# Performance work log

Hardware: AMD Instinct MI355X
Metric: run time of the kernel (lower is better)

The kernel has to match this reference:

```python
import jax, jax.numpy as jnp
import numpy as np
from jax import lax

B, C, H, W = 32, 684, 16, 64
HID, A, CK, K = 256, 512, 512, 11


def setup_inputs() -> dict:
    key = jax.random.key(0)
    ks = jax.random.split(key, 12)
    s = 0.02
    return {
        "cnn_features": jax.random.normal(ks[0], (B, C, H, W), jnp.float32),
        "hidden": jax.random.normal(ks[1], (B, HID), jnp.float32),
        "alpha_sum": jax.random.uniform(ks[2], (B, 1, H, W), jnp.float32),
        "image_mask": jnp.ones((B, 1, H, W), jnp.float32),
        # hidden_weight: Linear(HID -> A)
        "Wh": jax.random.normal(ks[3], (A, HID), jnp.float32) * s,
        "bh": jnp.zeros((A,), jnp.float32),
        # encoder_feature_conv: Conv2d(C -> A, 1x1) == pointwise linear
        "Wec": jax.random.normal(ks[4], (A, C), jnp.float32) * s,
        "bec": jnp.zeros((A,), jnp.float32),
        # attention_conv: Conv2d(1 -> CK, 11x11, pad 5, no bias)
        "Wac": jax.random.normal(ks[5], (CK, 1, K, K), jnp.float32) * s,
        # attention_weight: Linear(CK -> A, no bias)
        "Waw": jax.random.normal(ks[6], (A, CK), jnp.float32) * s,
        # alpha_convert: Linear(A -> 1)
        "Wv": jax.random.normal(ks[7], (1, A), jnp.float32) * s,
        "bv": jnp.zeros((1,), jnp.float32),
    }


def reference(cnn_features, hidden, alpha_sum, image_mask,
              Wh, bh, Wec, bec, Wac, Waw, Wv, bv):
    # query = hidden_weight(hidden): [B, A]
    query = hidden @ Wh.T + bh
    # attention_conv(alpha_sum): [B, CK, H, W]
    ast = lax.conv_general_dilated(
        alpha_sum, Wac, window_strides=(1, 1),
        padding=[(K // 2, K // 2), (K // 2, K // 2)],
        dimension_numbers=("NCHW", "OIHW", "NCHW"))
    # attention_weight on permuted conv output: [B, H, W, A]
    coverage_alpha = jnp.einsum("bkhw,ak->bhwa", ast, Waw)
    # encoder_feature_conv (1x1 conv == pointwise linear): [B, H, W, A]
    cnn_trans = jnp.einsum("bchw,ac->bhwa", cnn_features, Wec) + bec
    # additive attention score
    alpha_score = jnp.tanh(query[:, None, None, :] + coverage_alpha + cnn_trans)
    # alpha_convert -> scalar energy per position: [B, H, W]
    energy = jnp.einsum("bhwa,a->bhw", alpha_score, Wv[0]) + bv[0]
    energy = energy - energy.max()  # global max-subtract as in original
    energy_exp = jnp.exp(energy) * image_mask[:, 0]
    denom = energy_exp.sum(axis=(-1, -2))[:, None, None] + 1e-10
    alpha = energy_exp / denom  # [B, H, W]
    alpha_sum_new = alpha[:, None, :, :] + alpha_sum  # [B, 1, H, W]
    # context: weighted spatial sum over features -> [B, C]
    context_vector = jnp.einsum("bhw,bchw->bc", alpha, cnn_features)
    return (context_vector, alpha, alpha_sum_new)
```

## Files before the change

kernel.cpp:

```cpp
#include <hip/hip_runtime.h>
#include <math.h>

#define Bn   32
#define Cn   684
#define Hn   16
#define Wn   64
#define HWn  1024
#define HIDn 256
#define An   512
#define KKn  121
#define CREAL 805
#define CPAD 832
#define NSTEP 26

#define OUT_ALPHA 21888
#define OUT_ASUM  (21888 + 32768)

typedef short short8 __attribute__((ext_vector_type(8)));
typedef float floatx4 __attribute__((ext_vector_type(4)));

__device__ __forceinline__ unsigned short f2bf(float f) {
    union { float f; unsigned int i; } v; v.f = f;
    unsigned int i = v.i;
    return (unsigned short)((i + 0x7fffu + ((i >> 16) & 1u)) >> 16);
}

__device__ __forceinline__ void async_lds16(void* lds, const void* g) {
    __builtin_amdgcn_global_load_lds(
        (const __attribute__((address_space(1))) unsigned int*)g,
        (__attribute__((address_space(3))) unsigned int*)lds, 16, 0, 0);
}

__global__ __launch_bounds__(256) void k_query(
    const float* __restrict__ hidden,
    const float* __restrict__ Wh,
    const float* __restrict__ bh,
    const float* __restrict__ bec,
    float* __restrict__ query)
{
    __shared__ float hs[HIDn];
    const int b = blockIdx.x, t = threadIdx.x;
    if (t < HIDn) hs[t] = hidden[b * HIDn + t];
    __syncthreads();
    for (int a = t; a < An; a += 256) {
        const float4* wp = (const float4*)(Wh + (size_t)a * HIDn);
        float s = bh[a] + bec[a];
        #pragma unroll 8
        for (int i = 0; i < HIDn / 4; ++i) {
            float4 w = wp[i];
            s = fmaf(hs[4 * i],     w.x, s);
            s = fmaf(hs[4 * i + 1], w.y, s);
            s = fmaf(hs[4 * i + 2], w.z, s);
            s = fmaf(hs[4 * i + 3], w.w, s);
        }
        query[b * An + a] = s;
    }
}

__global__ __launch_bounds__(128) void k_build_vt(
    const float* __restrict__ Wec,
    const float* __restrict__ Wac,
    const float* __restrict__ Waw,
    unsigned short* __restrict__ VTbf)
{
    __shared__ float waw_s[512];
    const int a = blockIdx.x, t = threadIdx.x;
    for (int i = t; i < 512; i += 128) waw_s[i] = Waw[(size_t)a * 512 + i];
    __syncthreads();
    for (int cp = t; cp < Cn; cp += 128)
        VTbf[(size_t)a * CPAD + cp] = f2bf(Wec[(size_t)a * Cn + cp]);
    if (t < KKn) {
        float s = 0.f;
        #pragma unroll 8
        for (int k = 0; k < 512; ++k)
            s = fmaf(waw_s[k], Wac[k * KKn + t], s);
        VTbf[(size_t)a * CPAD + Cn + t] = f2bf(s);
    }
    for (int cp = CREAL + t; cp < CPAD; cp += 128)
        VTbf[(size_t)a * CPAD + cp] = 0;
}

__device__ __forceinline__ float fetchU(const float* __restrict__ X,
                                        const float* plane,
                                        int b, int hh, int m, int row) {
    if (row < Cn)   return X[((size_t)(b * Cn + row)) * HWn + hh * Wn + m];
    if (row < CREAL) {
        int ij = row - Cn; int di = ij / 11, dj = ij - di * 11;
        return plane[di * 74 + m + dj];
    }
    return 0.f;
}

__global__ __launch_bounds__(256, 2) void k_energy(
    const float* __restrict__ X,
    const float* __restrict__ asum,
    const float* __restrict__ Wv,
    const float* __restrict__ query,
    const unsigned short* __restrict__ VTbf,
    float* __restrict__ energy)
{
    __shared__ unsigned short As[64 * 40];
    __shared__ unsigned short Bs[512 * 32];
    __shared__ float plane[11 * 74];
    __shared__ float qs[512];
    __shared__ float wvs[512];

    const int t = threadIdx.x;
    const int hh = blockIdx.x, b = blockIdx.y;
    const int w = t >> 6, lane = t & 63;
    const int q = lane >> 4, r = lane & 15;

    for (int i = t; i < 11 * 74; i += 256) {
        int di = i / 74, cc = i - di * 74;
        int h2 = hh + di - 5, w2 = cc - 5;
        float v = 0.f;
        if (h2 >= 0 && h2 < Hn && w2 >= 0 && w2 < Wn) v = asum[b * HWn + h2 * Wn + w2];
        plane[i] = v;
    }
    qs[t]        = query[b * An + t];
    qs[t + 256]  = query[b * An + t + 256];
    wvs[t]       = Wv[t];
    wvs[t + 256] = Wv[t + 256];

    floatx4 acc[4][8];
    #pragma unroll
    for (int mf = 0; mf < 4; ++mf)
        #pragma unroll
        for (int nf = 0; nf < 8; ++nf)
            acc[mf][nf] = (floatx4){0.f, 0.f, 0.f, 0.f};

    for (int ch = 0; ch < NSTEP; ++ch) {
        const int c0 = ch * 32;
        __syncthreads();
        {
            unsigned int pk[4];
            #pragma unroll
            for (int jj = 0; jj < 4; ++jj) {
                int r0 = c0 + w * 8 + jj * 2;
                float v0 = fetchU(X, plane, b, hh, lane, r0);
                float v1 = fetchU(X, plane, b, hh, lane, r0 + 1);
                unsigned int u0 = __float_as_uint(v0), u1 = __float_as_uint(v1);
                u0 = (u0 + 0x7fffu + ((u0 >> 16) & 1u)) >> 16;
                u1 = (u1 + 0x7fffu + ((u1 >> 16) & 1u)) & 0xffff0000u;
                pk[jj] = u0 | u1;
            }
            uint4* dst = (uint4*)&As[lane * 40 + w * 8];
            *dst = make_uint4(pk[0], pk[1], pk[2], pk[3]);
        }
        #pragma unroll
        for (int ii = 0; ii < 8; ++ii) {
            int n0 = w * 128 + ii * 16;
            int rowB = n0 + (lane >> 2);
            int gc = (lane & 3) ^ ((lane >> 2) & 3);
            const unsigned short* gB = VTbf + (size_t)rowB * CPAD + c0 + gc * 8;
            async_lds16(&Bs[n0 * 32], gB);
        }
        __syncthreads();
        short8 af[4], bfr[8];
        #pragma unroll
        for (int mf = 0; mf < 4; ++mf)
            af[mf] = *(const short8*)&As[(mf * 16 + r) * 40 + q * 8];
        #pragma unroll
        for (int nf = 0; nf < 8; ++nf) {
            int rowB = w * 128 + nf * 16 + r;
            bfr[nf] = *(const short8*)&Bs[rowB * 32 + (q ^ (r & 3)) * 8];
        }
        #pragma unroll
        for (int mf = 0; mf < 4; ++mf)
            #pragma unroll
            for (int nf = 0; nf < 8; ++nf)
                acc[mf][nf] = __builtin_amdgcn_mfma_f32_16x16x32_bf16(
                    af[mf], bfr[nf], acc[mf][nf], 0, 0, 0);
    }

    float ep[16];
    #pragma unroll
    for (int i = 0; i < 16; ++i) ep[i] = 0.f;
    #pragma unroll
    for (int nf = 0; nf < 8; ++nf) {
        int n = w * 128 + nf * 16 + r;
        float qv = qs[n], wv = wvs[n];
        #pragma unroll
        for (int mf = 0; mf < 4; ++mf)
            #pragma unroll
            for (int rg = 0; rg < 4; ++rg) {
                float x = acc[mf][nf][rg] + qv;
                float e2 = __expf(2.f * x);
                float th = 1.f - 2.f * __builtin_amdgcn_rcpf(e2 + 1.f);
                ep[mf * 4 + rg] += wv * th;
            }
    }
    __syncthreads();
    float* red = (float*)Bs;
    #pragma unroll
    for (int mf = 0; mf < 4; ++mf)
        #pragma unroll
        for (int rg = 0; rg < 4; ++rg)
            red[(mf * 16 + q * 4 + rg) * 65 + w * 16 + r] = ep[mf * 4 + rg];
    __syncthreads();
    if (t < 64) {
        float s = 0.f;
        #pragma unroll 16
        for (int i = 0; i < 64; ++i) s += red[t * 65 + i];
        energy[b * HWn + hh * Wn + t] = s;
    }
}

__global__ __launch_bounds__(1024) void k_max(
    const float* __restrict__ energy, float* __restrict__ emax)
{
    __shared__ float wm[16];
    const int t = threadIdx.x;
    float m = -1e30f;
    for (int i = t; i < Bn * HWn; i += 1024) m = fmaxf(m, energy[i]);
    for (int off = 32; off >= 1; off >>= 1) m = fmaxf(m, __shfl_down(m, off, 64));
    if ((t & 63) == 0) wm[t >> 6] = m;
    __syncthreads();
    if (t == 0) {
        float mm = wm[0];
        for (int i = 1; i < 16; ++i) mm = fmaxf(mm, wm[i]);
        emax[0] = mm;
    }
}

__global__ __launch_bounds__(1024) void k_softmax(
    const float* __restrict__ energy, const float* __restrict__ emax,
    const float* __restrict__ mask, const float* __restrict__ asum,
    float* __restrict__ alpha_f, float* __restrict__ out)
{
    __shared__ float sm[17];
    const int b = blockIdx.x, t = threadIdx.x;
    float ex = expf(energy[b * HWn + t] - emax[0]) * mask[b * HWn + t];
    float s = ex;
    for (int off = 32; off >= 1; off >>= 1) s += __shfl_down(s, off, 64);
    if ((t & 63) == 0) sm[t >> 6] = s;
    __syncthreads();
    if (t == 0) {
        float tot = 0.f;
        for (int i = 0; i < 16; ++i) tot += sm[i];
        sm[16] = tot + 1e-10f;
    }
    __syncthreads();
    float alpha = ex / sm[16];
    alpha_f[b * HWn + t] = alpha;
    out[OUT_ALPHA + b * HWn + t] = alpha;
    out[OUT_ASUM  + b * HWn + t] = alpha + asum[b * HWn + t];
}

__global__ __launch_bounds__(256) void k_context(
    const float* __restrict__ X, const float* __restrict__ alpha_f,
    float* __restrict__ out)
{
    const int t = threadIdx.x, lane = t & 63, wid = t >> 6;
    const int b = blockIdx.y;
    const int c = blockIdx.x * 4 + wid;
    const float* xp = X + ((size_t)(b * Cn + c)) * HWn;
    const float* ap = alpha_f + b * HWn;
    float s = 0.f;
    #pragma unroll
    for (int i = 0; i < 4; ++i) {
        int off = i * 256 + lane * 4;
        float4 x = *(const float4*)(xp + off);
        float4 a = *(const float4*)(ap + off);
        s = fmaf(a.x, x.x, s);
        s = fmaf(a.y, x.y, s);
        s = fmaf(a.z, x.z, s);
        s = fmaf(a.w, x.w, s);
    }
    for (int off = 32; off >= 1; off >>= 1) s += __shfl_down(s, off, 64);
    if (lane == 0) out[b * Cn + c] = s;
}

extern "C" void kernel_launch(void* const* d_in, const int* in_sizes, int n_in,
                              void* d_out, int out_size, void* d_ws, size_t ws_size,
                              hipStream_t stream)
{
    const float* X      = (const float*)d_in[0];
    const float* hidden = (const float*)d_in[1];
    const float* asum   = (const float*)d_in[2];
    const float* mask   = (const float*)d_in[3];
    const float* Wh     = (const float*)d_in[4];
    const float* bh     = (const float*)d_in[5];
    const float* Wec    = (const float*)d_in[6];
    const float* bec    = (const float*)d_in[7];
    const float* Wac    = (const float*)d_in[8];
    const float* Waw    = (const float*)d_in[9];
    const float* Wv     = (const float*)d_in[10];
    (void)in_sizes; (void)n_in; (void)out_size; (void)ws_size;

    float* out = (float*)d_out;
    float* ws = (float*)d_ws;
    float* query   = ws;
    float* energy  = ws + 16384;
    float* emax    = ws + 16384 + 32768;
    float* alpha_f = emax + 16;
    unsigned short* VTbf = (unsigned short*)(alpha_f + 32768);

    k_query   <<<dim3(32),      dim3(256),  0, stream>>>(hidden, Wh, bh, bec, query);
    k_build_vt<<<dim3(512),     dim3(128),  0, stream>>>(Wec, Wac, Waw, VTbf);
    k_energy  <<<dim3(16, 32),  dim3(256),  0, stream>>>(X, asum, Wv, query, VTbf, energy);
    k_max     <<<dim3(1),       dim3(1024), 0, stream>>>(energy, emax);
    k_softmax <<<dim3(32),      dim3(1024), 0, stream>>>(energy, emax, mask, asum, alpha_f, out);
    k_context <<<dim3(171, 32), dim3(256),  0, stream>>>(X, alpha_f, out);
}
```

Measured before the change: 258.1 us.

## Drop LDS staging in energy GEMM, merge prep kernels, fuse max into softmax

The energy kernel now loads bf16 weight fragments and packed feature fragments straight from global memory into registers, with no LDS tiles and no per-step barriers. The loop is split so the fast path skips the coverage-plane branch. The query and weight-build kernels merge into one launch, and the separate global-max kernel is replaced by a per-batch max inside the softmax. Per-batch max subtraction is mathematically equivalent apart from epsilon and underflow effects. In exchange, each wave redundantly loads the whole feature tile with poorly coalesced strided loads and no prefetching.

```diff
diff --git a/kernel.cpp b/kernel.cpp
--- a/kernel.cpp
+++ b/kernel.cpp
@@ -24,71 +24,60 @@
     unsigned int i = v.i;
     return (unsigned short)((i + 0x7fffu + ((i >> 16) & 1u)) >> 16);
 }
-
-__device__ __forceinline__ void async_lds16(void* lds, const void* g) {
-    __builtin_amdgcn_global_load_lds(
-        (const __attribute__((address_space(1))) unsigned int*)g,
-        (__attribute__((address_space(3))) unsigned int*)lds, 16, 0, 0);
-}
-
-__global__ __launch_bounds__(256) void k_query(
+__device__ __forceinline__ unsigned int pack2bf(float v0, float v1) {
+    unsigned int u0 = __float_as_uint(v0), u1 = __float_as_uint(v1);
+    u0 = (u0 + 0x7fffu + ((u0 >> 16) & 1u)) >> 16;
+    u1 = (u1 + 0x7fffu + ((u1 >> 16) & 1u)) & 0xffff0000u;
+    return u0 | u1;
+}
+
+__global__ __launch_bounds__(256) void k_prep(
     const float* __restrict__ hidden,
     const float* __restrict__ Wh,
     const float* __restrict__ bh,
     const float* __restrict__ bec,
-    float* __restrict__ query)
-{
-    __shared__ float hs[HIDn];
-    const int b = blockIdx.x, t = threadIdx.x;
-    if (t < HIDn) hs[t] = hidden[b * HIDn + t];
-    __syncthreads();
-    for (int a = t; a < An; a += 256) {
-        const float4* wp = (const float4*)(Wh + (size_t)a * HIDn);
-        float s = bh[a] + bec[a];
-        #pragma unroll 8
-        for (int i = 0; i < HIDn / 4; ++i) {
-            float4 w = wp[i];
-            s = fmaf(hs[4 * i],     w.x, s);
-            s = fmaf(hs[4 * i + 1], w.y, s);
-            s = fmaf(hs[4 * i + 2], w.z, s);
-            s = fmaf(hs[4 * i + 3], w.w, s);
-        }
-        query[b * An + a] = s;
-    }
-}
-
-__global__ __launch_bounds__(128) void k_build_vt(
     const float* __restrict__ Wec,
     const float* __restrict__ Wac,
     const float* __restrict__ Waw,
+    float* __restrict__ query,
     unsigned short* __restrict__ VTbf)
 {
-    __shared__ float waw_s[512];
-    const int a = blockIdx.x, t = threadIdx.x;
-    for (int i = t; i < 512; i += 128) waw_s[i] = Waw[(size_t)a * 512 + i];
-    __syncthreads();
-    for (int cp = t; cp < Cn; cp += 128)
-        VTbf[(size_t)a * CPAD + cp] = f2bf(Wec[(size_t)a * Cn + cp]);
-    if (t < KKn) {
-        float s = 0.f;
-        #pragma unroll 8
-        for (int k = 0; k < 512; ++k)
-            s = fmaf(waw_s[k], Wac[k * KKn + t], s);
-        VTbf[(size_t)a * CPAD + Cn + t] = f2bf(s);
-    }
-    for (int cp = CREAL + t; cp < CPAD; cp += 128)
-        VTbf[(size_t)a * CPAD + cp] = 0;
-}
-
-__device__ __forceinline__ float fetchU(const float* __restrict__ X,
-                                        const float* plane,
-                                        int b, int hh, int m, int row) {
-    if (row < Cn)   return X[((size_t)(b * Cn + row)) * HWn + hh * Wn + m];
-    if (row < CREAL) {
-        int ij = row - Cn; int di = ij / 11, dj = ij - di * 11;
-        return plane[di * 74 + m + dj];
-    }
-    return 0.f;
+    __shared__ float sbuf[512];
+    const int blk = blockIdx.x, t = threadIdx.x;
+    if (blk < 512) {
+        const int a = blk;
+        sbuf[t]       = Waw[(size_t)a * 512 + t];
+        sbuf[t + 256] = Waw[(size_t)a * 512 + t + 256];
+        __syncthreads();
+        for (int cp = t; cp < Cn; cp += 256)
+            VTbf[(size_t)a * CPAD + cp] = f2bf(Wec[(size_t)a * Cn + cp]);
+        if (t < KKn) {
+            float s = 0.f;
+            #pragma unroll 8
+            for (int k = 0; k < 512; ++k)
+                s = fmaf(sbuf[k], Wac[k * KKn + t], s);
+            VTbf[(size_t)a * CPAD + Cn + t] = f2bf(s);
+        }
+        for (int cp = CREAL + t; cp < CPAD; cp += 256)
+            VTbf[(size_t)a * CPAD + cp] = 0;
+    } else {
+        const int b = blk - 512;
+        sbuf[t] = (t < HIDn) ? hidden[b * HIDn + t] : 0.f;
+        __syncthreads();
+        for (int a = t; a < An; a += 256) {
+            const float4* wp = (const float4*)(Wh + (size_t)a * HIDn);
+            float s = bh[a] + bec[a];
+            #pragma unroll 8
+            for (int i = 0; i < HIDn / 4; ++i) {
+                float4 w = wp[i];
+                s = fmaf(sbuf[4 * i],     w.x, s);
+                s = fmaf(sbuf[4 * i + 1], w.y, s);
+                s = fmaf(sbuf[4 * i + 2], w.z, s);
+                s = fmaf(sbuf[4 * i + 3], w.w, s);
+            }
+            query[b * An + a] = s;
+        }
+    }
 }
 
 __global__ __launch_bounds__(256, 2) void k_energy(
@@ -99,11 +88,10 @@
     const unsigned short* __restrict__ VTbf,
     float* __restrict__ energy)
 {
-    __shared__ unsigned short As[64 * 40];
-    __shared__ unsigned short Bs[512 * 32];
-    __shared__ float plane[11 * 74];
+    __shared__ float plane[11 * 74 + 2];
     __shared__ float qs[512];
     __shared__ float wvs[512];
+    __shared__ float red[64 * 65];
 
     const int t = threadIdx.x;
     const int hh = blockIdx.x, b = blockIdx.y;
@@ -114,13 +102,15 @@
         int di = i / 74, cc = i - di * 74;
         int h2 = hh + di - 5, w2 = cc - 5;
         float v = 0.f;
-        if (h2 >= 0 && h2 < Hn && w2 >= 0 && w2 < Wn) v = asum[b * HWn + h2 * Wn + w2];
+        if (h2 >= 0 && h2 < Hn && w2 >= 0 && w2 < Wn)
+            v = asum[b * HWn + h2 * Wn + w2];
         plane[i] = v;
     }
     qs[t]        = query[b * An + t];
     qs[t + 256]  = query[b * An + t + 256];
     wvs[t]       = Wv[t];
     wvs[t + 256] = Wv[t + 256];
+    __syncthreads();
 
     floatx4 acc[4][8];
     #pragma unroll
@@ -129,41 +119,65 @@
         for (int nf = 0; nf < 8; ++nf)
             acc[mf][nf] = (floatx4){0.f, 0.f, 0.f, 0.f};
 
-    for (int ch = 0; ch < NSTEP; ++ch) {
+    const float* Xb = X + (size_t)b * Cn * HWn + hh * Wn;
+    const unsigned short* Bb = VTbf + (size_t)(w * 128) * CPAD;
+
+    for (int ch = 0; ch < 21; ++ch) {
         const int c0 = ch * 32;
-        __syncthreads();
-        {
+        short8 bfr[8];
+        #pragma unroll
+        for (int nf = 0; nf < 8; ++nf)
+            bfr[nf] = *(const short8*)(Bb + (size_t)(nf * 16 + r) * CPAD + c0 + q * 8);
+        short8 af[4];
+        #pragma unroll
+        for (int mf = 0; mf < 4; ++mf) {
+            const int m = mf * 16 + r;
+            const float* xp = Xb + (size_t)(c0 + q * 8) * HWn + m;
             unsigned int pk[4];
             #pragma unroll
-            for (int jj = 0; jj < 4; ++jj) {
-                int r0 = c0 + w * 8 + jj * 2;
-                float v0 = fetchU(X, plane, b, hh, lane, r0);
-                float v1 = fetchU(X, plane, b, hh, lane, r0 + 1);
-                unsigned int u0 = __float_as_uint(v0), u1 = __float_as_uint(v1);
-                u0 = (u0 + 0x7fffu + ((u0 >> 16) & 1u)) >> 16;
-                u1 = (u1 + 0x7fffu + ((u1 >> 16) & 1u)) & 0xffff0000u;
-                pk[jj] = u0 | u1;
+            for (int jj = 0; jj < 4; ++jj)
+                pk[jj] = pack2bf(xp[(size_t)(2 * jj) * HWn], xp[(size_t)(2 * jj + 1) * HWn]);
+            union { unsigned int u[4]; short8 s; } cv;
+            cv.u[0] = pk[0]; cv.u[1] = pk[1]; cv.u[2] = pk[2]; cv.u[3] = pk[3];
+            af[mf] = cv.s;
+        }
+        #pragma unroll
+        for (int mf = 0; mf < 4; ++mf)
+            #pragma unroll
+            for (int nf = 0; nf < 8; ++nf)
+                acc[mf][nf] = __builtin_amdgcn_mfma_f32_16x16x32_bf16(
+                    af[mf], bfr[nf], acc[mf][nf], 0, 0, 0);
+    }
+    for (int ch = 21; ch < NSTEP; ++ch) {
+        const int c0 = ch * 32;
+        short8 bfr[8];
+        #pragma unroll
+        for (int nf = 0; nf < 8; ++nf)
+            bfr[nf] = *(const short8*)(Bb + (size_t)(nf * 16 + r) * CPAD + c0 + q * 8);
+        short8 af[4];
+        #pragma unroll
+        for (int mf = 0; mf < 4; ++mf) {
+            const int m = mf * 16 + r;
+            float v[8];
+            #pragma unroll
+            for (int jj = 0; jj < 8; ++jj) {
+                int row = c0 + q * 8 + jj;
+                float x;
+                if (row < Cn) {
+                    x = Xb[(size_t)row * HWn + m];
+                } else if (row < CREAL) {
+                    int ij = row - Cn; int di = ij / 11, dj = ij - di * 11;
+                    x = plane[di * 74 + m + dj];
+                } else {
+                    x = 0.f;
+                }
+                v[jj] = x;
             }
-            uint4* dst = (uint4*)&As[lane * 40 + w * 8];
-            *dst = make_uint4(pk[0], pk[1], pk[2], pk[3]);
-        }
-        #pragma unroll
-        for (int ii = 0; ii < 8; ++ii) {
-            int n0 = w * 128 + ii * 16;
-            int rowB = n0 + (lane >> 2);
-            int gc = (lane & 3) ^ ((lane >> 2) & 3);
-            const unsigned short* gB = VTbf + (size_t)rowB * CPAD + c0 + gc * 8;
-            async_lds16(&Bs[n0 * 32], gB);
-        }
-        __syncthreads();
-        short8 af[4], bfr[8];
-        #pragma unroll
-        for (int mf = 0; mf < 4; ++mf)
-            af[mf] = *(const short8*)&As[(mf * 16 + r) * 40 + q * 8];
-        #pragma unroll
-        for (int nf = 0; nf < 8; ++nf) {
-            int rowB = w * 128 + nf * 16 + r;
-            bfr[nf] = *(const short8*)&Bs[rowB * 32 + (q ^ (r & 3)) * 8];
+            union { unsigned int u[4]; short8 s; } cv;
+            #pragma unroll
+            for (int jj = 0; jj < 4; ++jj)
+                cv.u[jj] = pack2bf(v[2 * jj], v[2 * jj + 1]);
+            af[mf] = cv.s;
         }
         #pragma unroll
         for (int mf = 0; mf < 4; ++mf)
@@ -191,7 +205,6 @@
             }
     }
     __syncthreads();
-    float* red = (float*)Bs;
     #pragma unroll
     for (int mf = 0; mf < 4; ++mf)
         #pragma unroll
@@ -206,42 +219,38 @@
     }
 }
 
-__global__ __launch_bounds__(1024) void k_max(
-    const float* __restrict__ energy, float* __restrict__ emax)
-{
-    __shared__ float wm[16];
-    const int t = threadIdx.x;
-    float m = -1e30f;
-    for (int i = t; i < Bn * HWn; i += 1024) m = fmaxf(m, energy[i]);
-    for (int off = 32; off >= 1; off >>= 1) m = fmaxf(m, __shfl_down(m, off, 64));
-    if ((t & 63) == 0) wm[t >> 6] = m;
-    __syncthreads();
-    if (t == 0) {
-        float mm = wm[0];
-        for (int i = 1; i < 16; ++i) mm = fmaxf(mm, wm[i]);
-        emax[0] = mm;
-    }
-}
-
 __global__ __launch_bounds__(1024) void k_softmax(
-    const float* __restrict__ energy, const float* __restrict__ emax,
+    const float* __restrict__ energy,
     const float* __restrict__ mask, const float* __restrict__ asum,
     float* __restrict__ alpha_f, float* __restrict__ out)
 {
-    __shared__ float sm[17];
+    __shared__ float sm[16];
+    __shared__ float bc[2];
     const int b = blockIdx.x, t = threadIdx.x;
-    float ex = expf(energy[b * HWn + t] - emax[0]) * mask[b * HWn + t];
+    float e = energy[b * HWn + t];
+    float m = e;
+    for (int off = 32; off >= 1; off >>= 1) m = fmaxf(m, __shfl_down(m, off, 64));
+    if ((t & 63) == 0) sm[t >> 6] = m;
+    __syncthreads();
+    if (t == 0) {
+        float mm = sm[0];
+        for (int i = 1; i < 16; ++i) mm = fmaxf(mm, sm[i]);
+        bc[0] = mm;
+    }
+    __syncthreads();
+    float ex = expf(e - bc[0]) * mask[b * HWn + t];
     float s = ex;
     for (int off = 32; off >= 1; off >>= 1) s += __shfl_down(s, off, 64);
+    __syncthreads();
     if ((t & 63) == 0) sm[t >> 6] = s;
     __syncthreads();
     if (t == 0) {
         float tot = 0.f;
         for (int i = 0; i < 16; ++i) tot += sm[i];
-        sm[16] = tot + 1e-10f;
-    }
-    __syncthreads();
-    float alpha = ex / sm[16];
+        bc[1] = tot + 1e-10f;
+    }
+    __syncthreads();
+    float alpha = ex / bc[1];
     alpha_f[b * HWn + t] = alpha;
     out[OUT_ALPHA + b * HWn + t] = alpha;
     out[OUT_ASUM  + b * HWn + t] = alpha + asum[b * HWn + t];
@@ -292,14 +301,12 @@
     float* ws = (float*)d_ws;
     float* query   = ws;
     float* energy  = ws + 16384;
-    float* emax    = ws + 16384 + 32768;
-    float* alpha_f = emax + 16;
-    unsigned short* VTbf = (unsigned short*)(alpha_f + 32768);
-
-    k_query   <<<dim3(32),      dim3(256),  0, stream>>>(hidden, Wh, bh, bec, query);
-    k_build_vt<<<dim3(512),     dim3(128),  0, stream>>>(Wec, Wac, Waw, VTbf);
+    float* alpha_f = ws + 16384 + 32768;
+    unsigned short* VTbf = (unsigned short*)(ws + 81920);
+
+    k_prep    <<<dim3(544),     dim3(256),  0, stream>>>(hidden, Wh, bh, bec,
+                                                         Wec, Wac, Waw, query, VTbf);
     k_energy  <<<dim3(16, 32),  dim3(256),  0, stream>>>(X, asum, Wv, query, VTbf, energy);
-    k_max     <<<dim3(1),       dim3(1024), 0, stream>>>(energy, emax);
-    k_softmax <<<dim3(32),      dim3(1024), 0, stream>>>(energy, emax, mask, asum, alpha_f, out);
+    k_softmax <<<dim3(32),      dim3(1024), 0, stream>>>(energy, mask, asum, alpha_f, out);
     k_context <<<dim3(171, 32), dim3(256),  0, stream>>>(X, alpha_f, out);
 }
```

After: 270.9 us. 5.0% more time.
